# Performance work log

Measured on AMD Instinct MI355X. Metric: run time of the kernel, lower is better.

The kernel has to match this reference:

```python
import jax, jax.numpy as jnp
import numpy as np
from jax import lax

B, T, DEPTH = 512, 32, 512
RNN, NCC = 512, 128
D_IN = DEPTH * (T * DEPTH // T // DEPTH) * 1 + NCC  # slice_len=1 -> 512 + 128 = 640


def setup_inputs() -> dict:
    key = jax.random.key(0)
    ks = jax.random.split(key, 7)
    s = 0.05  # tf.random_normal_initializer default stddev
    return {
        "f_pool": jax.random.normal(ks[0], (B, T, DEPTH), jnp.float32),
        "ground_truth": jax.random.normal(ks[1], (B, T, NCC), jnp.float32),
        "kernel": jax.random.normal(ks[2], (DEPTH + NCC, 4 * RNN), jnp.float32) * s,
        "rec_kernel": jax.random.normal(ks[3], (RNN, 4 * RNN), jnp.float32) * s,
        "bias": jax.random.normal(ks[4], (4 * RNN,), jnp.float32) * s,
        "softmax_w": jax.random.normal(ks[5], (RNN, NCC), jnp.float32) * s,
        "softmax_b": jax.random.normal(ks[6], (NCC,), jnp.float32) * s,
    }


def reference(f_pool, ground_truth, kernel, rec_kernel, bias, softmax_w, softmax_b):
    b, features_num, depth = f_pool.shape
    seq_length = ground_truth.shape[1]
    ncc = softmax_b.shape[0]
    rnn = rec_kernel.shape[0]
    slice_len = features_num // seq_length  # == 1 here
    gt_t = jnp.transpose(ground_truth, (1, 0, 2))  # [T, B, C] for scan

    def step(carry, inp):
        h, c, prev = carry
        t, gt_row = inp
        # image feature slice at char index t -> [B, slice_len*depth]
        feat = lax.dynamic_slice_in_dim(f_pool, t, slice_len, axis=1)
        feat = feat.reshape(b, slice_len * depth)
        x = jnp.concatenate([feat, prev], axis=1)
        z = x @ kernel + h @ rec_kernel + bias  # [B, 4*rnn]
        i, f, g, o = jnp.split(z, 4, axis=1)    # keras LSTMCell gate order
        c2 = jax.nn.sigmoid(f) * c + jax.nn.sigmoid(i) * jnp.tanh(g)
        h2 = jax.nn.sigmoid(o) * jnp.tanh(c2)
        logits = h2 @ softmax_w + softmax_b
        onehot = jax.nn.one_hot(jnp.argmax(logits, axis=1), ncc, dtype=f_pool.dtype)
        # teacher forcing: prev_output = ground_truth[:, t, :]
        return (h2, c2, gt_row), onehot

    h0 = jnp.zeros((b, rnn), f_pool.dtype)
    c0 = jnp.zeros((b, rnn), f_pool.dtype)
    prev0 = jnp.zeros((b, ncc), f_pool.dtype)
    (h, c, _), outs = lax.scan(step, (h0, c0, prev0), (jnp.arange(seq_length), gt_t))
    sequence_output = jnp.transpose(outs, (1, 0, 2))  # [B, T, C]
    return (sequence_output, h, c)
```

## Files before the change

kernel.cpp:

```cpp
#include <hip/hip_runtime.h>
#include <math.h>

typedef float  f32x4  __attribute__((ext_vector_type(4)));
typedef short  short8v __attribute__((ext_vector_type(8)));
typedef unsigned short ushort8v __attribute__((ext_vector_type(8)));
typedef unsigned short ushort2v __attribute__((ext_vector_type(2)));

#define KP_PRE 3840
#define KP_HS  1536

#define WAITV(N) asm volatile("s_waitcnt vmcnt(" #N ")" ::: "memory")
#define SBAR()   asm volatile("s_barrier" ::: "memory")

__device__ unsigned short g_Xb[16384][3840];
__device__ unsigned short g_Wb[2048][3840];
__device__ unsigned short g_Rb[2048][1536];
__device__ unsigned short g_hs[2][512][1536];
__device__ float g_pre[16384][2048];
__device__ float g_hf[2][512 * 512];
__device__ float g_swT[128][512];
__device__ float g_bperm[2048];
__device__ float g_plv[2][512 * 8];
__device__ int   g_pli[2][512 * 8];
__device__ unsigned g_xcnt[128];
__device__ unsigned g_xrel[128];

__global__ void init_counters()
{
    int t = threadIdx.x;
    if (t < 8) { g_xcnt[t * 16] = 0u; g_xrel[t * 16] = 0u; }
}

__device__ __forceinline__ unsigned short f2bf(float f) {
    unsigned u = __float_as_uint(f);
    return (unsigned short)((u + 0x7fffu + ((u >> 16) & 1u)) >> 16);
}
__device__ __forceinline__ float bf2f(unsigned short s) {
    return __uint_as_float(((unsigned)s) << 16);
}
__device__ __forceinline__ float sigf(float x) { return 1.f / (1.f + expf(-x)); }

__device__ __forceinline__ void split3(float v, unsigned short& s0,
                                       unsigned short& s1, unsigned short& s2) {
    s0 = f2bf(v); float f0 = bf2f(s0);
    s1 = f2bf(v - f0); float f1 = bf2f(s1);
    s2 = f2bf(v - f0 - f1);
}

__device__ __constant__ int c_ipt[6] = {0, 0, 1, 0, 1, 2};
__device__ __constant__ int c_jpt[6] = {0, 1, 0, 2, 1, 0};

__device__ __forceinline__ void gl16(const unsigned short* g, unsigned short* l) {
    __builtin_amdgcn_global_load_lds((const __attribute__((address_space(1))) void*)g,
                                     (__attribute__((address_space(3))) void*)l, 16, 0, 0);
}

__device__ __forceinline__ short8v fragld(const unsigned short* sh, int row, int uw) {
    return *(const short8v*)(sh + row * 64 + ((uw ^ (row & 7)) << 3));
}

template<int AUNITS, int BUNITS>
__device__ __forceinline__ void stage_chunk(const unsigned short* Ag, int pitchA,
                                            const unsigned short* Bg, int pitchB,
                                            int kb, unsigned short* slot, int tid)
{
#pragma unroll
    for (int v = 0; v < AUNITS / 256; ++v) {
        int e = v * 256 + tid;
        gl16(Ag + (size_t)(e >> 3) * pitchA + kb * 64 + (e & 7) * 8, slot + e * 8);
    }
#pragma unroll
    for (int v = 0; v < BUNITS / 256; ++v) {
        int e = v * 256 + tid;
        gl16(Bg + (size_t)(e >> 3) * pitchB + kb * 64 + (e & 7) * 8,
             slot + AUNITS * 8 + e * 8);
    }
}

__device__ __forceinline__ void stageA3w(const unsigned short* Ag, int kr,
                                         unsigned short* buf, int tid)
{
#pragma unroll
    for (int s = 0; s < 3; ++s) {
        int e = tid;
        gl16(Ag + (size_t)(e >> 3) * KP_HS + (s * 8 + kr) * 64 + (e & 7) * 8,
             buf + s * 4096 + e * 8);
    }
}
__device__ __forceinline__ void stageB3w(const unsigned short* Bg, int kr,
                                         unsigned short* buf, int tid)
{
#pragma unroll
    for (int s = 0; s < 3; ++s) {
        int e = tid;
        gl16(Bg + (size_t)(e >> 3) * KP_HS + (s * 8 + kr) * 64 + (e & 7) * 8,
             buf + 12288 + s * 4096 + e * 8);
    }
}
__device__ __forceinline__ void stage6w(const unsigned short* Ag,
                                        const unsigned short* Bg,
                                        int kr, unsigned short* buf, int tid)
{
    stageA3w(Ag, kr, buf, tid);
    stageB3w(Bg, kr, buf, tid);
}

__global__ __launch_bounds__(256) void build_Xb(const float* __restrict__ fp,
                                                const float* __restrict__ gt)
{
    const int tid = threadIdx.x;
    const int m  = blockIdx.x * 16 + (tid >> 4);
    const int k8 = (blockIdx.y * 16 + (tid & 15)) * 8;
    const int t = m >> 9, b = m & 511;
    float x[8];
    if (k8 < 512) {
        float4 v0 = *(const float4*)(fp + ((size_t)(b * 32 + t)) * 512 + k8);
        float4 v1 = *(const float4*)(fp + ((size_t)(b * 32 + t)) * 512 + k8 + 4);
        x[0]=v0.x; x[1]=v0.y; x[2]=v0.z; x[3]=v0.w;
        x[4]=v1.x; x[5]=v1.y; x[6]=v1.z; x[7]=v1.w;
    } else if (t > 0) {
        float4 v0 = *(const float4*)(gt + ((size_t)(b * 32 + t - 1)) * 128 + (k8 - 512));
        float4 v1 = *(const float4*)(gt + ((size_t)(b * 32 + t - 1)) * 128 + (k8 - 512) + 4);
        x[0]=v0.x; x[1]=v0.y; x[2]=v0.z; x[3]=v0.w;
        x[4]=v1.x; x[5]=v1.y; x[6]=v1.z; x[7]=v1.w;
    } else {
#pragma unroll
        for (int j = 0; j < 8; ++j) x[j] = 0.f;
    }
    unsigned short s0[8], s1[8], s2[8];
#pragma unroll
    for (int j = 0; j < 8; ++j) split3(x[j], s0[j], s1[j], s2[j]);
    const int u = (k8 >> 3) & 7;
    const int base = (k8 & ~63) + (((u ^ (m & 7))) << 3);
#pragma unroll
    for (int p = 0; p < 6; ++p) {
        ushort8v v;
#pragma unroll
        for (int j = 0; j < 8; ++j)
            v[j] = (c_ipt[p] == 0) ? s0[j] : ((c_ipt[p] == 1) ? s1[j] : s2[j]);
        *(ushort8v*)&g_Xb[m][p * 640 + base] = v;
    }
}

__global__ __launch_bounds__(256) void build_Wb(const float* __restrict__ Wk)
{
    const int tid = threadIdx.x;
    const int np = blockIdx.x * 16 + (tid >> 4);
    const int k8 = (blockIdx.y * 16 + (tid & 15)) * 8;
    const int n = (np & 3) * 512 + (np >> 2);
    float x[8];
#pragma unroll
    for (int j = 0; j < 8; ++j) x[j] = Wk[(size_t)(k8 + j) * 2048 + n];
    unsigned short s0[8], s1[8], s2[8];
#pragma unroll
    for (int j = 0; j < 8; ++j) split3(x[j], s0[j], s1[j], s2[j]);
    const int u = (k8 >> 3) & 7;
    const int base = (k8 & ~63) + (((u ^ (np & 7))) << 3);
#pragma unroll
    for (int p = 0; p < 6; ++p) {
        ushort8v v;
#pragma unroll
        for (int j = 0; j < 8; ++j)
            v[j] = (c_jpt[p] == 0) ? s0[j] : ((c_jpt[p] == 1) ? s1[j] : s2[j]);
        *(ushort8v*)&g_Wb[np][p * 640 + base] = v;
    }
}

__global__ __launch_bounds__(256) void build_Rb(const float* __restrict__ Rk)
{
    const int tid = threadIdx.x;
    const int np = blockIdx.x * 16 + (tid >> 4);
    const int k8 = (blockIdx.y * 16 + (tid & 15)) * 8;
    const int n = (np & 3) * 512 + (np >> 2);
    float x[8];
#pragma unroll
    for (int j = 0; j < 8; ++j) x[j] = Rk[(size_t)(k8 + j) * 2048 + n];
    unsigned short s0[8], s1[8], s2[8];
#pragma unroll
    for (int j = 0; j < 8; ++j) split3(x[j], s0[j], s1[j], s2[j]);
    const int u = (k8 >> 3) & 7;
    const int base = (k8 & ~63) + (((u ^ (np & 7))) << 3);
    ushort8v v0, v1, v2;
#pragma unroll
    for (int j = 0; j < 8; ++j) { v0[j] = s0[j]; v1[j] = s1[j]; v2[j] = s2[j]; }
    *(ushort8v*)&g_Rb[np][0 * 512 + base] = v0;
    *(ushort8v*)&g_Rb[np][1 * 512 + base] = v1;
    *(ushort8v*)&g_Rb[np][2 * 512 + base] = v2;
}

__global__ __launch_bounds__(256) void build_misc(const float* __restrict__ sw,
                                                  const float* __restrict__ bias)
{
    int id = blockIdx.x * 256 + threadIdx.x;
    if (id < 128 * 512) {
        int c = id >> 9, r = id & 511;
        g_swT[c][r] = sw[(size_t)r * 128 + c];
    } else if (id < 128 * 512 + 2048) {
        int np = id - 128 * 512;
        g_bperm[np] = bias[(np & 3) * 512 + (np >> 2)];
    }
}

__global__ __launch_bounds__(256, 1) void pre_mfma()
{
    __shared__ __align__(16) char smem[98304];
    const int tid = threadIdx.x, lane = tid & 63, wave = tid >> 6;
    const int n0 = blockIdx.x * 64, m0 = blockIdx.y * 128;
    const int wr = wave >> 1, wc = wave & 1, l15 = lane & 15, ql = lane >> 4;
    unsigned short* ring = (unsigned short*)smem;
    const unsigned short* Ag = &g_Xb[m0][0];
    const unsigned short* Bg = &g_Wb[n0][0];

    f32x4 acc[4][2];
#pragma unroll
    for (int a = 0; a < 4; ++a)
#pragma unroll
        for (int b = 0; b < 2; ++b) acc[a][b] = (f32x4){0.f, 0.f, 0.f, 0.f};

    stage_chunk<1024, 512>(Ag, KP_PRE, Bg, KP_PRE, 0, ring + 0 * 12288, tid);
    stage_chunk<1024, 512>(Ag, KP_PRE, Bg, KP_PRE, 1, ring + 1 * 12288, tid);
    stage_chunk<1024, 512>(Ag, KP_PRE, Bg, KP_PRE, 2, ring + 2 * 12288, tid);
    for (int c = 0; c < 60; ++c) {
        if (c <= 57)      WAITV(12);
        else if (c == 58) WAITV(6);
        else              WAITV(0);
        SBAR();
        const unsigned short* Ac = ring + (c & 3) * 12288;
        const unsigned short* Bc = Ac + 8192;
#pragma unroll
        for (int sub = 0; sub < 2; ++sub) {
            const int uw = sub * 4 + ql;
            short8v af[4], bfr[2];
#pragma unroll
            for (int fa = 0; fa < 4; ++fa)
                af[fa] = fragld(Ac, wr * 64 + fa * 16 + l15, uw);
#pragma unroll
            for (int fb = 0; fb < 2; ++fb)
                bfr[fb] = fragld(Bc, wc * 32 + fb * 16 + l15, uw);
#pragma unroll
            for (int fa = 0; fa < 4; ++fa)
#pragma unroll
                for (int fb = 0; fb < 2; ++fb)
                    acc[fa][fb] = __builtin_amdgcn_mfma_f32_16x16x32_bf16(
                        af[fa], bfr[fb], acc[fa][fb], 0, 0, 0);
        }
        if (c + 3 < 60)
            stage_chunk<1024, 512>(Ag, KP_PRE, Bg, KP_PRE, c + 3,
                                   ring + ((c + 3) & 3) * 12288, tid);
    }
#pragma unroll
    for (int fa = 0; fa < 4; ++fa)
#pragma unroll
        for (int fb = 0; fb < 2; ++fb) {
            const int np = n0 + wc * 32 + fb * 16 + l15;
            const float bv = g_bperm[np];
#pragma unroll
            for (int q = 0; q < 4; ++q) {
                const int m = m0 + wr * 64 + fa * 16 + ql * 4 + q;
                g_pre[m][np] = acc[fa][fb][q] + bv;
            }
        }
}

__global__ __launch_bounds__(512, 1) void charnn_rec(
    const float* __restrict__ sb,
    float* __restrict__ seq, float* __restrict__ out_h, float* __restrict__ out_c)
{
    __shared__ __align__(16) char smem[147456];
    float (*zbuf)[68] = (float (*)[68])smem;
    unsigned short* ring = (unsigned short*)smem;

    const int bi = blockIdx.x, tid = threadIdx.x;
    const int lane = tid & 63, wave = tid >> 6;
    const int x  = bi & 7, jj = bi >> 3;
    const int Mg = x;
    const int Ng = jj;
    const int m0 = Mg * 64, n0 = Ng * 64;
    const int wr = wave >> 2, wc = wave & 3, l15 = lane & 15, ql = lane >> 4;

    const int m_e = tid >> 3;
    const int rb2 = (tid & 7) * 2;
    const int mg = m0 + m_e;
    float cst[2] = {0.f, 0.f};

    const int rgrp = Mg * 4 + (jj & 3);
    const int cg   = jj >> 2;
    const int arow = Mg * 64 + jj * 2;
    const bool xleader = (jj == 0);

    constexpr int ipt[6] = {0, 0, 1, 0, 1, 2};
    constexpr int jpt[6] = {0, 1, 0, 2, 1, 0};

    const unsigned short* Bg = &g_Rb[n0][0];

    f32x4 pqa, pqb;
    {
        const float* prow = &g_pre[0 * 512 + mg][n0];
        pqa = *(const f32x4*)(prow + rb2 * 4);
        pqb = *(const f32x4*)(prow + rb2 * 4 + 4);
    }

    for (int ph = 0; ph < 34; ++ph) {
        const int t = ph;
        const bool do_z = (ph >= 1 && ph <= 31);

        const unsigned short* Ag = nullptr;
        if (do_z) {
            Ag = &g_hs[(t + 1) & 1][m0][0];
            stageA3w(Ag, 0, ring + 0 * 24576, tid);
            stageA3w(Ag, 1, ring + 1 * 24576, tid);
            stageA3w(Ag, 2, ring + 2 * 24576, tid);
        }

        if (ph >= 1 && ph <= 32 && tid < 256) {
            const int tl = ph - 1;
            const int row = rgrp * 16 + (tid >> 4);
            const int col = cg * 16 + (tid & 15);
            const float* hrow = &g_hf[tl & 1][(size_t)row * 512];
            const float* wcol = &g_swT[col][0];
            float s0 = sb[col], s1 = 0.f, s2 = 0.f, s3 = 0.f;
#pragma unroll 8
            for (int k = 0; k < 512; k += 4) {
                float4 hv = *(const float4*)(hrow + k);
                float4 wv = *(const float4*)(wcol + k);
                s0 = fmaf(hv.x, wv.x, s0); s1 = fmaf(hv.y, wv.y, s1);
                s2 = fmaf(hv.z, wv.z, s2); s3 = fmaf(hv.w, wv.w, s3);
            }
            float bv = (s0 + s1) + (s2 + s3); int bidx = col;
#pragma unroll
            for (int m = 1; m < 16; m <<= 1) {
                float ov = __shfl_xor(bv, m, 64);
                int   oi = __shfl_xor(bidx, m, 64);
                if (ov > bv || (ov == bv && oi < bidx)) { bv = ov; bidx = oi; }
            }
            if ((tid & 15) == 0) {
                g_plv[tl & 1][row * 8 + cg] = bv;
                g_pli[tl & 1][row * 8 + cg] = bidx;
            }
        }

        if (ph >= 2 && wave < 2) {
            const int t2 = ph - 2;
            const int row = arow + wave;
            float v; int idx;
            if (lane < 8) {
                v   = g_plv[t2 & 1][row * 8 + lane];
                idx = g_pli[t2 & 1][row * 8 + lane];
            } else { v = -INFINITY; idx = 0x7fffffff; }
#pragma unroll
            for (int m = 1; m < 8; m <<= 1) {
                float ov = __shfl_xor(v, m, 64);
                int   oi = __shfl_xor(idx, m, 64);
                if (ov > v || (ov == v && oi < idx)) { v = ov; idx = oi; }
            }
            int win = __shfl(idx, 0, 64);
            if (lane < 32) {
                int c4 = lane * 4;
                float4 o;
                o.x = (c4 + 0 == win) ? 1.f : 0.f;
                o.y = (c4 + 1 == win) ? 1.f : 0.f;
                o.z = (c4 + 2 == win) ? 1.f : 0.f;
                o.w = (c4 + 3 == win) ? 1.f : 0.f;
                *(float4*)(seq + ((size_t)row * 32 + t2) * 128 + c4) = o;
            }
        }

        if (ph <= 31) {
            if (do_z) {
                f32x4 acc[2];
                acc[0] = (f32x4){0.f, 0.f, 0.f, 0.f};
                acc[1] = (f32x4){0.f, 0.f, 0.f, 0.f};
#pragma unroll
                for (int kr = 0; kr < 8; ++kr) {
                    if (kr >= 1 && kr <= 5)
                        stage6w(Ag, Bg, kr + 2, ring + ((kr + 2) % 3) * 24576, tid);
                    if      (kr == 0) WAITV(6);
                    else if (kr == 1) WAITV(9);
                    else if (kr == 6) WAITV(6);
                    else if (kr == 7) WAITV(0);
                    else              WAITV(12);
                    SBAR();
                    const unsigned short* Ab = ring + (kr % 3) * 24576;
                    const unsigned short* Bb = Ab + 12288;
#pragma unroll
                    for (int sub = 0; sub < 2; ++sub) {
                        const int uw = sub * 4 + ql;
                        short8v a0[2], a1[2], a2[2], b0, b1, b2;
                        a0[0] = fragld(Ab + 0 * 4096, wr * 32 + l15, uw);
                        a0[1] = fragld(Ab + 0 * 4096, wr * 32 + 16 + l15, uw);
                        a1[0] = fragld(Ab + 1 * 4096, wr * 32 + l15, uw);
                        a1[1] = fragld(Ab + 1 * 4096, wr * 32 + 16 + l15, uw);
                        a2[0] = fragld(Ab + 2 * 4096, wr * 32 + l15, uw);
                        a2[1] = fragld(Ab + 2 * 4096, wr * 32 + 16 + l15, uw);
                        b0 = fragld(Bb + 0 * 4096, wc * 16 + l15, uw);
                        b1 = fragld(Bb + 1 * 4096, wc * 16 + l15, uw);
                        b2 = fragld(Bb + 2 * 4096, wc * 16 + l15, uw);
#pragma unroll
                        for (int p = 0; p < 6; ++p) {
                            const short8v* A2 = (ipt[p] == 0) ? a0 :
                                                ((ipt[p] == 1) ? a1 : a2);
                            const short8v  B2 = (jpt[p] == 0) ? b0 :
                                                ((jpt[p] == 1) ? b1 : b2);
                            acc[0] = __builtin_amdgcn_mfma_f32_16x16x32_bf16(
                                A2[0], B2, acc[0], 0, 0, 0);
                            acc[1] = __builtin_amdgcn_mfma_f32_16x16x32_bf16(
                                A2[1], B2, acc[1], 0, 0, 0);
                        }
                    }
                }
                __syncthreads();
#pragma unroll
                for (int fa = 0; fa < 2; ++fa)
#pragma unroll
                    for (int q2 = 0; q2 < 4; ++q2)
                        zbuf[wr * 32 + fa * 16 + ql * 4 + q2]
                            [wc * 16 + l15] = acc[fa][q2];
            }
            __syncthreads();

            unsigned short hs0[2], hs1[2], hs2[2];
            float hv2[2];
#pragma unroll
            for (int i = 0; i < 2; ++i) {
                const int rl = rb2 + i;
                float zi, zf, zg, zo;
                if (t > 0) {
                    float4 zq = *(const float4*)&zbuf[m_e][rl * 4];
                    zi = zq.x; zf = zq.y; zg = zq.z; zo = zq.w;
                } else { zi = zf = zg = zo = 0.f; }
                f32x4 pq = (i == 0) ? pqa : pqb;
                zi += pq[0]; zf += pq[1]; zg += pq[2]; zo += pq[3];
                float c2 = sigf(zf) * cst[i] + sigf(zi) * tanhf(zg);
                float h2 = sigf(zo) * tanhf(c2);
                cst[i] = c2;
                hv2[i] = h2;
                split3(h2, hs0[i], hs1[i], hs2[i]);
            }
            const int r0g = Ng * 16 + rb2;
            *(float2*)&g_hf[t & 1][(size_t)mg * 512 + r0g] =
                make_float2(hv2[0], hv2[1]);
            if (t == 31) {
                *(float2*)&out_h[(size_t)mg * 512 + r0g] =
                    make_float2(hv2[0], hv2[1]);
                *(float2*)&out_c[(size_t)mg * 512 + r0g] =
                    make_float2(cst[0], cst[1]);
            }
            const int su = ((r0g >> 3) & 7) ^ (mg & 7);
            const int abase = (r0g & ~63) + (su << 3) + (r0g & 7);
#pragma unroll
            for (int i = 0; i < 3; ++i) {
                ushort2v v;
#pragma unroll
                for (int j = 0; j < 2; ++j)
                    v[j] = (i == 0) ? hs0[j] : ((i == 1) ? hs1[j] : hs2[j]);
                *(ushort2v*)&g_hs[t & 1][mg][i * 512 + abase] = v;
            }
        }

        if (ph < 33) {
            __syncthreads();

            if (ph <= 30) {
                stageB3w(Bg, 0, ring + 0 * 24576, tid);
                stageB3w(Bg, 1, ring + 1 * 24576, tid);
                stageB3w(Bg, 2, ring + 2 * 24576, tid);
                const float* prow = &g_pre[(ph + 1) * 512 + mg][n0];
                pqa = *(const f32x4*)(prow + rb2 * 4);
                pqb = *(const f32x4*)(prow + rb2 * 4 + 4);
            }

            if (tid == 0) {
                __hip_atomic_fetch_add(&g_xcnt[x * 16], 1u,
                                       __ATOMIC_RELAXED, __HIP_MEMORY_SCOPE_AGENT);
                if (xleader) {
                    const unsigned xt = 32u * (unsigned)(ph + 1);
                    while (__hip_atomic_load(&g_xcnt[x * 16], __ATOMIC_RELAXED,
                                             __HIP_MEMORY_SCOPE_AGENT) < xt)
                        __builtin_amdgcn_s_sleep(2);
                    __hip_atomic_store(&g_xrel[x * 16], (unsigned)(ph + 1),
                                       __ATOMIC_RELAXED, __HIP_MEMORY_SCOPE_AGENT);
                }
                while (__hip_atomic_load(&g_xrel[x * 16], __ATOMIC_RELAXED,
                                         __HIP_MEMORY_SCOPE_AGENT) < (unsigned)(ph + 1))
                    __builtin_amdgcn_s_sleep(2);
                __builtin_amdgcn_fence(__ATOMIC_ACQUIRE, "agent");
            }
            __syncthreads();
        }
    }
}

extern "C" void kernel_launch(void* const* d_in, const int* in_sizes, int n_in,
                              void* d_out, int out_size, void* d_ws, size_t ws_size,
                              hipStream_t stream)
{
    const float* fp   = (const float*)d_in[0];
    const float* gt   = (const float*)d_in[1];
    const float* Wk   = (const float*)d_in[2];
    const float* Rk   = (const float*)d_in[3];
    const float* bias = (const float*)d_in[4];
    const float* sw   = (const float*)d_in[5];
    const float* sb   = (const float*)d_in[6];
    float* seq   = (float*)d_out;
    float* out_h = seq + (size_t)512 * 32 * 128;
    float* out_c = out_h + (size_t)512 * 512;

    hipLaunchKernelGGL(init_counters, dim3(1), dim3(64), 0, stream);
    hipLaunchKernelGGL(build_Xb, dim3(1024, 5), dim3(256), 0, stream, fp, gt);
    hipLaunchKernelGGL(build_Wb, dim3(128, 5), dim3(256), 0, stream, Wk);
    hipLaunchKernelGGL(build_Rb, dim3(128, 4), dim3(256), 0, stream, Rk);
    hipLaunchKernelGGL(build_misc, dim3(264), dim3(256), 0, stream, sw, bias);
    hipLaunchKernelGGL(pre_mfma, dim3(32, 128), dim3(256), 0, stream);
    hipLaunchKernelGGL(charnn_rec, dim3(256), dim3(512), 0, stream,
                       sb, seq, out_h, out_c);
}
```

Measured before the change: 1.643 ms.

## Remap blocks so each XCD pair shares a 128-row group with pairwise barrier

After: 1.698 ms. 1.03x slower.

```diff
diff --git a/kernel.cpp b/kernel.cpp
--- a/kernel.cpp
+++ b/kernel.cpp
@@ -2,6 +2,7 @@
 #include <math.h>
 
 typedef float  f32x4  __attribute__((ext_vector_type(4)));
+typedef float  f32x2  __attribute__((ext_vector_type(2)));
 typedef short  short8v __attribute__((ext_vector_type(8)));
 typedef unsigned short ushort8v __attribute__((ext_vector_type(8)));
 typedef unsigned short ushort2v __attribute__((ext_vector_type(2)));
@@ -23,12 +24,14 @@
 __device__ float g_plv[2][512 * 8];
 __device__ int   g_pli[2][512 * 8];
 __device__ unsigned g_xcnt[128];
-__device__ unsigned g_xrel[128];
+__device__ unsigned g_pcnt[256];
+__device__ unsigned g_prel[256];
 
 __global__ void init_counters()
 {
     int t = threadIdx.x;
-    if (t < 8) { g_xcnt[t * 16] = 0u; g_xrel[t * 16] = 0u; }
+    if (t < 8) g_xcnt[t * 16] = 0u;
+    if (t < 4) { g_pcnt[t * 64] = 0u; g_prel[t * 64] = 0u; }
 }
 
 __device__ __forceinline__ unsigned short f2bf(float f) {
@@ -273,8 +276,9 @@
     const int bi = blockIdx.x, tid = threadIdx.x;
     const int lane = tid & 63, wave = tid >> 6;
     const int x  = bi & 7, jj = bi >> 3;
-    const int Mg = x;
-    const int Ng = jj;
+    const int P  = x >> 1, e = x & 1;
+    const int Mg = 2 * P + (jj & 1);
+    const int Ng = e * 16 + (jj >> 1);
     const int m0 = Mg * 64, n0 = Ng * 64;
     const int wr = wave >> 2, wc = wave & 3, l15 = lane & 15, ql = lane >> 4;
 
@@ -283,10 +287,12 @@
     const int mg = m0 + m_e;
     float cst[2] = {0.f, 0.f};
 
-    const int rgrp = Mg * 4 + (jj & 3);
-    const int cg   = jj >> 2;
-    const int arow = Mg * 64 + jj * 2;
+    const int q    = e * 32 + jj;
+    const int rgrp = 8 * P + (q & 7);
+    const int cg   = q >> 3;
+    const int arow = 128 * P + q * 2;
     const bool xleader = (jj == 0);
+    const bool pleader = (jj == 0 && e == 0);
 
     constexpr int ipt[6] = {0, 0, 1, 0, 1, 2};
     constexpr int jpt[6] = {0, 1, 0, 2, 1, 0};
@@ -334,8 +340,8 @@
                 if (ov > bv || (ov == bv && oi < bidx)) { bv = ov; bidx = oi; }
             }
             if ((tid & 15) == 0) {
-                g_plv[tl & 1][row * 8 + cg] = bv;
-                g_pli[tl & 1][row * 8 + cg] = bidx;
+                __builtin_nontemporal_store(bv,   &g_plv[tl & 1][row * 8 + cg]);
+                __builtin_nontemporal_store(bidx, &g_pli[tl & 1][row * 8 + cg]);
             }
         }
 
@@ -437,8 +443,11 @@
                 split3(h2, hs0[i], hs1[i], hs2[i]);
             }
             const int r0g = Ng * 16 + rb2;
-            *(float2*)&g_hf[t & 1][(size_t)mg * 512 + r0g] =
-                make_float2(hv2[0], hv2[1]);
+            {
+                f32x2 hv = {hv2[0], hv2[1]};
+                __builtin_nontemporal_store(
+                    hv, (f32x2*)&g_hf[t & 1][(size_t)mg * 512 + r0g]);
+            }
             if (t == 31) {
                 *(float2*)&out_h[(size_t)mg * 512 + r0g] =
                     make_float2(hv2[0], hv2[1]);
@@ -453,7 +462,8 @@
 #pragma unroll
                 for (int j = 0; j < 2; ++j)
                     v[j] = (i == 0) ? hs0[j] : ((i == 1) ? hs1[j] : hs2[j]);
-                *(ushort2v*)&g_hs[t & 1][mg][i * 512 + abase] = v;
+                __builtin_nontemporal_store(
+                    v, (ushort2v*)&g_hs[t & 1][mg][i * 512 + abase]);
             }
         }
 
@@ -477,10 +487,19 @@
                     while (__hip_atomic_load(&g_xcnt[x * 16], __ATOMIC_RELAXED,
                                              __HIP_MEMORY_SCOPE_AGENT) < xt)
                         __builtin_amdgcn_s_sleep(2);
-                    __hip_atomic_store(&g_xrel[x * 16], (unsigned)(ph + 1),
-                                       __ATOMIC_RELAXED, __HIP_MEMORY_SCOPE_AGENT);
+                    __builtin_amdgcn_fence(__ATOMIC_RELEASE, "agent");
+                    __hip_atomic_fetch_add(&g_pcnt[P * 64], 1u,
+                                           __ATOMIC_RELAXED, __HIP_MEMORY_SCOPE_AGENT);
+                    if (pleader) {
+                        const unsigned pt = 2u * (unsigned)(ph + 1);
+                        while (__hip_atomic_load(&g_pcnt[P * 64], __ATOMIC_RELAXED,
+                                                 __HIP_MEMORY_SCOPE_AGENT) < pt)
+                            __builtin_amdgcn_s_sleep(2);
+                        __hip_atomic_store(&g_prel[P * 64], (unsigned)(ph + 1),
+                                           __ATOMIC_RELAXED, __HIP_MEMORY_SCOPE_AGENT);
+                    }
                 }
-                while (__hip_atomic_load(&g_xrel[x * 16], __ATOMIC_RELAXED,
+                while (__hip_atomic_load(&g_prel[P * 64], __ATOMIC_RELAXED,
                                          __HIP_MEMORY_SCOPE_AGENT) < (unsigned)(ph + 1))
                     __builtin_amdgcn_s_sleep(2);
                 __builtin_amdgcn_fence(__ATOMIC_ACQUIRE, "agent");
```

## Store three bf16 splits once and form six split products in registers

Applied to the files above, without the earlier changes.

After: 1.458 ms. 11.2% less time.

```diff
diff --git a/kernel.cpp b/kernel.cpp
--- a/kernel.cpp
+++ b/kernel.cpp
@@ -6,14 +6,14 @@
 typedef unsigned short ushort8v __attribute__((ext_vector_type(8)));
 typedef unsigned short ushort2v __attribute__((ext_vector_type(2)));
 
-#define KP_PRE 3840
+#define KP_PRE 1920
 #define KP_HS  1536
 
 #define WAITV(N) asm volatile("s_waitcnt vmcnt(" #N ")" ::: "memory")
 #define SBAR()   asm volatile("s_barrier" ::: "memory")
 
-__device__ unsigned short g_Xb[16384][3840];
-__device__ unsigned short g_Wb[2048][3840];
+__device__ unsigned short g_Xb[16384][1920];
+__device__ unsigned short g_Wb[2048][1920];
 __device__ unsigned short g_Rb[2048][1536];
 __device__ unsigned short g_hs[2][512][1536];
 __device__ float g_pre[16384][2048];
@@ -47,9 +47,6 @@
     s2 = f2bf(v - f0 - f1);
 }
 
-__device__ __constant__ int c_ipt[6] = {0, 0, 1, 0, 1, 2};
-__device__ __constant__ int c_jpt[6] = {0, 1, 0, 2, 1, 0};
-
 __device__ __forceinline__ void gl16(const unsigned short* g, unsigned short* l) {
     __builtin_amdgcn_global_load_lds((const __attribute__((address_space(1))) void*)g,
                                      (__attribute__((address_space(3))) void*)l, 16, 0, 0);
@@ -59,22 +56,26 @@
     return *(const short8v*)(sh + row * 64 + ((uw ^ (row & 7)) << 3));
 }
 
-template<int AUNITS, int BUNITS>
-__device__ __forceinline__ void stage_chunk(const unsigned short* Ag, int pitchA,
-                                            const unsigned short* Bg, int pitchB,
-                                            int kb, unsigned short* slot, int tid)
-{
-#pragma unroll
-    for (int v = 0; v < AUNITS / 256; ++v) {
-        int e = v * 256 + tid;
-        gl16(Ag + (size_t)(e >> 3) * pitchA + kb * 64 + (e & 7) * 8, slot + e * 8);
-    }
-#pragma unroll
-    for (int v = 0; v < BUNITS / 256; ++v) {
-        int e = v * 256 + tid;
-        gl16(Bg + (size_t)(e >> 3) * pitchB + kb * 64 + (e & 7) * 8,
-             slot + AUNITS * 8 + e * 8);
-    }
+__device__ __forceinline__ void stage_pre(const unsigned short* Ag,
+                                          const unsigned short* Bg,
+                                          int kr, unsigned short* slot, int tid)
+{
+#pragma unroll
+    for (int s = 0; s < 3; ++s)
+#pragma unroll
+        for (int v = 0; v < 4; ++v) {
+            int e = v * 256 + tid;
+            gl16(Ag + (size_t)(e >> 3) * KP_PRE + s * 640 + kr * 64 + (e & 7) * 8,
+                 slot + s * 8192 + e * 8);
+        }
+#pragma unroll
+    for (int s = 0; s < 3; ++s)
+#pragma unroll
+        for (int v = 0; v < 2; ++v) {
+            int e = v * 256 + tid;
+            gl16(Bg + (size_t)(e >> 3) * KP_PRE + s * 640 + kr * 64 + (e & 7) * 8,
+                 slot + 24576 + s * 4096 + e * 8);
+        }
 }
 
 __device__ __forceinline__ void stageA3w(const unsigned short* Ag, int kr,
@@ -132,14 +133,12 @@
     for (int j = 0; j < 8; ++j) split3(x[j], s0[j], s1[j], s2[j]);
     const int u = (k8 >> 3) & 7;
     const int base = (k8 & ~63) + (((u ^ (m & 7))) << 3);
-#pragma unroll
-    for (int p = 0; p < 6; ++p) {
-        ushort8v v;
-#pragma unroll
-        for (int j = 0; j < 8; ++j)
-            v[j] = (c_ipt[p] == 0) ? s0[j] : ((c_ipt[p] == 1) ? s1[j] : s2[j]);
-        *(ushort8v*)&g_Xb[m][p * 640 + base] = v;
-    }
+    ushort8v v0, v1, v2;
+#pragma unroll
+    for (int j = 0; j < 8; ++j) { v0[j] = s0[j]; v1[j] = s1[j]; v2[j] = s2[j]; }
+    *(ushort8v*)&g_Xb[m][0 * 640 + base] = v0;
+    *(ushort8v*)&g_Xb[m][1 * 640 + base] = v1;
+    *(ushort8v*)&g_Xb[m][2 * 640 + base] = v2;
 }
 
 __global__ __launch_bounds__(256) void build_Wb(const float* __restrict__ Wk)
@@ -156,14 +155,12 @@
     for (int j = 0; j < 8; ++j) split3(x[j], s0[j], s1[j], s2[j]);
     const int u = (k8 >> 3) & 7;
     const int base = (k8 & ~63) + (((u ^ (np & 7))) << 3);
-#pragma unroll
-    for (int p = 0; p < 6; ++p) {
-        ushort8v v;
-#pragma unroll
-        for (int j = 0; j < 8; ++j)
-            v[j] = (c_jpt[p] == 0) ? s0[j] : ((c_jpt[p] == 1) ? s1[j] : s2[j]);
-        *(ushort8v*)&g_Wb[np][p * 640 + base] = v;
-    }
+    ushort8v v0, v1, v2;
+#pragma unroll
+    for (int j = 0; j < 8; ++j) { v0[j] = s0[j]; v1[j] = s1[j]; v2[j] = s2[j]; }
+    *(ushort8v*)&g_Wb[np][0 * 640 + base] = v0;
+    *(ushort8v*)&g_Wb[np][1 * 640 + base] = v1;
+    *(ushort8v*)&g_Wb[np][2 * 640 + base] = v2;
 }
 
 __global__ __launch_bounds__(256) void build_Rb(const float* __restrict__ Rk)
@@ -203,50 +200,65 @@
 
 __global__ __launch_bounds__(256, 1) void pre_mfma()
 {
-    __shared__ __align__(16) char smem[98304];
+    __shared__ __align__(16) char smem[147456];
     const int tid = threadIdx.x, lane = tid & 63, wave = tid >> 6;
-    const int n0 = blockIdx.x * 64, m0 = blockIdx.y * 128;
+    const int vid = blockIdx.y * 32 + blockIdx.x;
+    const int x8 = vid & 7, k = vid >> 3;
+    const int m0 = (x8 + 8 * (k >> 5)) * 128;
+    const int n0 = (k & 31) * 64;
     const int wr = wave >> 1, wc = wave & 1, l15 = lane & 15, ql = lane >> 4;
     unsigned short* ring = (unsigned short*)smem;
     const unsigned short* Ag = &g_Xb[m0][0];
     const unsigned short* Bg = &g_Wb[n0][0];
 
+    constexpr int ipt[6] = {0, 0, 1, 0, 1, 2};
+    constexpr int jpt[6] = {0, 1, 0, 2, 1, 0};
+
     f32x4 acc[4][2];
 #pragma unroll
     for (int a = 0; a < 4; ++a)
 #pragma unroll
         for (int b = 0; b < 2; ++b) acc[a][b] = (f32x4){0.f, 0.f, 0.f, 0.f};
 
-    stage_chunk<1024, 512>(Ag, KP_PRE, Bg, KP_PRE, 0, ring + 0 * 12288, tid);
-    stage_chunk<1024, 512>(Ag, KP_PRE, Bg, KP_PRE, 1, ring + 1 * 12288, tid);
-    stage_chunk<1024, 512>(Ag, KP_PRE, Bg, KP_PRE, 2, ring + 2 * 12288, tid);
-    for (int c = 0; c < 60; ++c) {
-        if (c <= 57)      WAITV(12);
-        else if (c == 58) WAITV(6);
-        else              WAITV(0);
+    stage_pre(Ag, Bg, 0, ring, tid);
+    stage_pre(Ag, Bg, 1, ring + 36864, tid);
+    for (int kr = 0; kr < 10; ++kr) {
+        if (kr <= 8) WAITV(18);
+        else         WAITV(0);
         SBAR();
-        const unsigned short* Ac = ring + (c & 3) * 12288;
-        const unsigned short* Bc = Ac + 8192;
+        const unsigned short* Ab = ring + (kr & 1) * 36864;
+        const unsigned short* Bb = Ab + 24576;
 #pragma unroll
         for (int sub = 0; sub < 2; ++sub) {
             const int uw = sub * 4 + ql;
-            short8v af[4], bfr[2];
-#pragma unroll
-            for (int fa = 0; fa < 4; ++fa)
-                af[fa] = fragld(Ac, wr * 64 + fa * 16 + l15, uw);
-#pragma unroll
-            for (int fb = 0; fb < 2; ++fb)
-                bfr[fb] = fragld(Bc, wc * 32 + fb * 16 + l15, uw);
-#pragma unroll
-            for (int fa = 0; fa < 4; ++fa)
-#pragma unroll
-                for (int fb = 0; fb < 2; ++fb)
-                    acc[fa][fb] = __builtin_amdgcn_mfma_f32_16x16x32_bf16(
-                        af[fa], bfr[fb], acc[fa][fb], 0, 0, 0);
-        }
-        if (c + 3 < 60)
-            stage_chunk<1024, 512>(Ag, KP_PRE, Bg, KP_PRE, c + 3,
-                                   ring + ((c + 3) & 3) * 12288, tid);
+            short8v a0[4], a1[4], a2[4], b0[2], b1[2], b2[2];
+#pragma unroll
+            for (int fa = 0; fa < 4; ++fa) {
+                a0[fa] = fragld(Ab + 0 * 8192, wr * 64 + fa * 16 + l15, uw);
+                a1[fa] = fragld(Ab + 1 * 8192, wr * 64 + fa * 16 + l15, uw);
+                a2[fa] = fragld(Ab + 2 * 8192, wr * 64 + fa * 16 + l15, uw);
+            }
+#pragma unroll
+            for (int fb = 0; fb < 2; ++fb) {
+                b0[fb] = fragld(Bb + 0 * 4096, wc * 32 + fb * 16 + l15, uw);
+                b1[fb] = fragld(Bb + 1 * 4096, wc * 32 + fb * 16 + l15, uw);
+                b2[fb] = fragld(Bb + 2 * 4096, wc * 32 + fb * 16 + l15, uw);
+            }
+#pragma unroll
+            for (int p = 0; p < 6; ++p) {
+                const short8v* A2 = (ipt[p] == 0) ? a0 : ((ipt[p] == 1) ? a1 : a2);
+                const short8v* B2 = (jpt[p] == 0) ? b0 : ((jpt[p] == 1) ? b1 : b2);
+#pragma unroll
+                for (int fa = 0; fa < 4; ++fa)
+#pragma unroll
+                    for (int fb = 0; fb < 2; ++fb)
+                        acc[fa][fb] = __builtin_amdgcn_mfma_f32_16x16x32_bf16(
+                            A2[fa], B2[fb], acc[fa][fb], 0, 0, 0);
+            }
+        }
+        SBAR();
+        if (kr + 2 < 10)
+            stage_pre(Ag, Bg, kr + 2, ring + (kr & 1) * 36864, tid);
     }
 #pragma unroll
     for (int fa = 0; fa < 4; ++fa)
```
